# Optimization experiments

Hardware: AMD Instinct MI355X
Metric: run time of the kernel (lower is better)

## Reference

```python
import jax, jax.numpy as jnp
import numpy as np

MODES = 16  # FourierLayer default


def _fourier_layer(h, w):
    # h: [B, S, H] real; w: [H, H, MODES] complex
    S = h.shape[1]
    h_ft = jnp.fft.rfft(h, axis=1)                 # [B, F, H] complex, F = S//2+1
    m = min(MODES, h_ft.shape[1])
    # batched complex matmul over the retained low-frequency modes
    out_m = jnp.einsum('bmh,hkm->bmk', h_ft[:, :m, :], w[:, :, :m])
    out_ft = jnp.zeros_like(h_ft).at[:, :m, :].set(out_m)  # higher modes zeroed
    h = jnp.fft.irfft(out_ft, n=S, axis=1)
    return jax.nn.gelu(h, approximate=False)       # torch nn.GELU() is exact erf


def setup_inputs() -> dict:
    key = jax.random.key(0)
    ks = jax.random.split(key, 7)
    B, S, H, L = 32, 8192, 128, 4
    x = jax.random.normal(ks[0], (B, S), jnp.float32)
    proj_w = jax.random.normal(ks[1], (H,), jnp.float32)          # Linear(1,H).weight[:,0]
    proj_b = jax.random.normal(ks[2], (H,), jnp.float32) * 0.02
    w_re = jax.random.normal(ks[3], (L, H, H, MODES), jnp.float32) * 0.02
    w_im = jax.random.normal(ks[4], (L, H, H, MODES), jnp.float32) * 0.02
    out_w = jax.random.normal(ks[5], (H,), jnp.float32) * 0.02    # Linear(H,1).weight[0]
    out_b = jax.random.normal(ks[6], (1,), jnp.float32) * 0.02
    return {"x": x, "proj_w": proj_w, "proj_b": proj_b,
            "w_re": w_re, "w_im": w_im, "out_w": out_w, "out_b": out_b}


def reference(x, proj_w, proj_b, w_re, w_im, out_w, out_b):
    # projection: Linear(1, H) applied to x.unsqueeze(-1)
    h = x[..., None] * proj_w + proj_b            # [B, S, H]
    W = (w_re + 1j * w_im).astype(jnp.complex64)  # [L, H, H, MODES]
    for l in range(w_re.shape[0]):                # fixed small layer count
        h = _fourier_layer(h, W[l])
    # output projection Linear(H, 1) then squeeze(-1)
    return h @ out_w + out_b[0]                   # [B, S]
```

## Files before the change

kernel.cpp:

```cpp
#include <hip/hip_runtime.h>
#include <hip/hip_bf16.h>

#define S_LEN 8192
#define NH 128
#define NM 16
#define NB 32
#define NBATCH 32
#define GP2 136
#define C2PI 6.2831853071795864769f

typedef __hip_bfloat16 bf16;
typedef unsigned short ushort_t;
typedef unsigned int uint_t;

typedef __bf16 bf16x8 __attribute__((ext_vector_type(8)));
typedef float floatx4 __attribute__((ext_vector_type(4)));

__device__ __forceinline__ float b2f(bf16 v){ return __bfloat162float(v); }
__device__ __forceinline__ float ldf(const void* p, long i, int f32){
    return f32 ? ((const float*)p)[i] : b2f(((const bf16*)p)[i]);
}
__device__ __forceinline__ float gelu_fast(float x){
    float z = fabsf(x) * 0.70710678118654752440f;
    float t = __builtin_amdgcn_rcpf(__builtin_fmaf(0.3275911f, z, 1.0f));
    float p = t*(0.254829592f + t*(-0.284496736f + t*(1.421413741f +
              t*(-1.453152027f + t*1.061405429f))));
    float e = __expf(-z * z);
    float er = __builtin_fmaf(-p, e, 1.0f);
    float s = copysignf(er, x);
    return 0.5f * x * (1.0f + s);
}
__device__ __forceinline__ ushort_t f2us(float v){
    return __builtin_bit_cast(ushort_t, (__bf16)v);
}
__device__ __forceinline__ void split_bf(float v, ushort_t& hi, ushort_t& lo){
    __bf16 h = (__bf16)v;
    float r = v - (float)h;
    hi = __builtin_bit_cast(ushort_t, h);
    lo = __builtin_bit_cast(ushort_t, (__bf16)r);
}
__device__ __forceinline__ bf16x8 ld8(const ushort_t* p){
    return *(const bf16x8*)(const void*)p;
}
__device__ __forceinline__ floatx4 MF(bf16x8 a, bf16x8 b, floatx4 c){
    return __builtin_amdgcn_mfma_f32_16x16x32_bf16(a, b, c, 0, 0, 0);
}

__device__ __forceinline__ int detect_f32(const void* x, int tid){
    __shared__ int sflag;
    if (tid < 64){
        const ushort_t* p = (const ushort_t*)x;
        int cnt = 0;
        for (int i = tid; i < 4096; i += 64){
            int e = (p[i] >> 7) & 0xFF;
            if (e >= 0xA0) cnt++;
        }
        #pragma unroll
        for (int off = 32; off > 0; off >>= 1) cnt += __shfl_xor(cnt, off, 64);
        if (tid == 0) sflag = (cnt > 400) ? 1 : 0;
    }
    __syncthreads();
    return sflag;
}

__device__ __forceinline__ void c_prologue(const float* __restrict__ C,
                                           int b, int c, int q,
                                           bf16x8* Bhi, bf16x8* Blo){
    const float* Cb = C + (long)b * NB * NH;
    #pragma unroll
    for (int kt = 0; kt < 8; kt++){
        int k = kt * 16 + c;
        bf16x8 h8, l8;
        #pragma unroll
        for (int e = 0; e < 8; e++){
            int j = 8 * q + e;
            float sc = (j == 0) ? (1.0f / S_LEN)
                     : (j < NM) ? (2.0f / S_LEN)
                     : (j == NM) ? 0.f : (-2.0f / S_LEN);
            float v = Cb[j * NH + k] * sc;
            __bf16 hh = (__bf16)v;
            h8[e] = hh;
            l8[e] = (__bf16)(v - (float)hh);
        }
        Bhi[kt] = h8; Blo[kt] = l8;
    }
}

__global__ __launch_bounds__(256) void k_prep(const void* __restrict__ x,
                                              const void* __restrict__ pw,
                                              const void* __restrict__ pb,
                                              float* __restrict__ M,
                                              ushort_t* __restrict__ Thi,
                                              ushort_t* __restrict__ Tlo,
                                              ushort_t* __restrict__ TThi,
                                              float* __restrict__ C0){
    int bid = blockIdx.x;
    int tid = threadIdx.x;
    if (bid < 512){
        int f32 = detect_f32(x, tid);
        int m = bid >> 5, b = bid & 31;
        float re = 0.f, im = 0.f;
        for (int s = tid; s < S_LEN; s += 256){
            float xv = ldf(x, (long)b * S_LEN + s, f32);
            float cv = 1.f, sv = 0.f;
            if (m != 0){
                int r = (m * s) & (S_LEN - 1);
                float th = (float)r * (C2PI / (float)S_LEN);
                sincosf(th, &sv, &cv);
            }
            re += xv * cv;
            im -= xv * sv;
        }
        __shared__ float sre[256], sim[256];
        sre[tid] = re; sim[tid] = im;
        __syncthreads();
        for (int off = 128; off > 0; off >>= 1){
            if (tid < off){ sre[tid] += sre[tid + off]; sim[tid] += sim[tid + off]; }
            __syncthreads();
        }
        if (tid < NH){
            float Xre = sre[0], Xim = sim[0];
            int h = tid;
            float pwv = ldf(pw, h, f32);
            float fc = pwv * Xre + (m == 0 ? (float)S_LEN * ldf(pb, h, f32) : 0.f);
            float fs = -pwv * Xim;
            M[(long)b * NB * NH + m * NH + h]        = fc;
            M[(long)b * NB * NH + (NM + m) * NH + h] = fs;
        }
    } else {
        int bb = bid - 512;
        int s = bb * 16 + (tid >> 4);
        int m = tid & 15;
        float cv = 1.f, sv = 0.f;
        if (m != 0){
            int r = (m * s) & (S_LEN - 1);
            float th = (float)r * (C2PI / (float)S_LEN);
            sincosf(th, &sv, &cv);
        }
        ushort_t chi, clo, shi, slo;
        split_bf(cv, chi, clo);
        split_bf(sv, shi, slo);
        Thi[s * NB + m] = chi;       Tlo[s * NB + m] = clo;
        Thi[s * NB + NM + m] = shi;  Tlo[s * NB + NM + m] = slo;
        TThi[m * S_LEN + s] = chi;
        TThi[(NM + m) * S_LEN + s] = shi;
        C0[bb * 256 + tid] = 0.f;
    }
}

__global__ __launch_bounds__(256) void k_mixA(const void* __restrict__ x,
                                              float* __restrict__ M,
                                              const void* __restrict__ wre,
                                              const void* __restrict__ wim,
                                              long woff,
                                              float* __restrict__ C){
    int tid = threadIdx.x;
    int f32 = detect_f32(x, tid);
    int hc = blockIdx.x, b = blockIdx.y;
    int k = tid & 127, mh = tid >> 7;
    int m0 = mh * 8;
    int h0 = hc * 16;
    __shared__ float Ms[NB * 16];
    for (int i = tid; i < NB * 16; i += 256){
        int j = i >> 4, hh = i & 15;
        Ms[j * 16 + hh] = M[(long)b * NB * NH + j * NH + h0 + hh];
    }
    __syncthreads();
    for (int i = tid; i < NB * 16; i += 256){
        int j = i >> 4, hh = i & 15;
        M[(long)b * NB * NH + j * NH + h0 + hh] = 0.f;
    }
    float Cr[8] = {0,0,0,0,0,0,0,0}, Ci[8] = {0,0,0,0,0,0,0,0};
    #pragma unroll 4
    for (int hh = 0; hh < 16; hh++){
        long base = woff + ((long)(h0 + hh) * NH + k) * NM + m0;
        float wr[8], wi[8];
        if (f32){
            const float4* wr4 = (const float4*)((const float*)wre + base);
            const float4* wi4 = (const float4*)((const float*)wim + base);
            float4 a0 = wr4[0], a1 = wr4[1], c0 = wi4[0], c1 = wi4[1];
            wr[0]=a0.x; wr[1]=a0.y; wr[2]=a0.z; wr[3]=a0.w;
            wr[4]=a1.x; wr[5]=a1.y; wr[6]=a1.z; wr[7]=a1.w;
            wi[0]=c0.x; wi[1]=c0.y; wi[2]=c0.z; wi[3]=c0.w;
            wi[4]=c1.x; wi[5]=c1.y; wi[6]=c1.z; wi[7]=c1.w;
        } else {
            bf16x8 a = ld8((const ushort_t*)wre + base);
            bf16x8 c = ld8((const ushort_t*)wim + base);
            #pragma unroll
            for (int e = 0; e < 8; e++){ wr[e] = (float)a[e]; wi[e] = (float)c[e]; }
        }
        #pragma unroll
        for (int e = 0; e < 8; e++){
            float fc = Ms[(m0 + e) * 16 + hh];
            float fs = Ms[(NM + m0 + e) * 16 + hh];
            Cr[e] += fc * wr[e] + fs * wi[e];
            Ci[e] += fc * wi[e] - fs * wr[e];
        }
    }
    float* Cb = C + (long)b * NB * NH;
    #pragma unroll
    for (int e = 0; e < 8; e++){
        atomicAdd(&Cb[(m0 + e) * NH + k],      Cr[e]);
        atomicAdd(&Cb[(NM + m0 + e) * NH + k], Ci[e]);
    }
}

__global__ __launch_bounds__(256, 4) void k_fused(const ushort_t* __restrict__ Thi,
                                                  const ushort_t* __restrict__ Tlo,
                                                  const ushort_t* __restrict__ TThi,
                                                  const float* __restrict__ C,
                                                  float* __restrict__ Cnext,
                                                  float* __restrict__ M){
    int b = blockIdx.y;
    int sx = blockIdx.x;
    int s0 = sx * 256;
    int tid = threadIdx.x;
    int w = tid >> 6;
    int lane = tid & 63;
    int c = lane & 15, q = lane >> 4;
    __shared__ ushort_t Glds[NH * GP2];

    bf16x8 Bhi[8], Blo[8];
    c_prologue(C, b, c, q, Bhi, Blo);
    if (tid < 32){
        *(float4*)(Cnext + (long)b * NB * NH + sx * 128 + tid * 4)
            = (float4){0.f, 0.f, 0.f, 0.f};
    }
    floatx4 a00 = {0,0,0,0}, a01 = {0,0,0,0}, a10 = {0,0,0,0}, a11 = {0,0,0,0};
    int kt0 = 2 * w;
    for (int p = 0; p < 2; p++){
        int sp = s0 + p * 128;
        #pragma unroll
        for (int sti = 0; sti < 2; sti++){
            int st = w * 2 + sti;
            long ar = (long)(sp + st * 16 + c) * NB + 8 * q;
            bf16x8 Ahi = ld8(Thi + ar);
            bf16x8 Alo = ld8(Tlo + ar);
            #pragma unroll
            for (int kt = 0; kt < 8; kt++){
                floatx4 acc = {0.f, 0.f, 0.f, 0.f};
                acc = MF(Ahi, Bhi[kt], acc);
                acc = MF(Alo, Bhi[kt], acc);
                acc = MF(Ahi, Blo[kt], acc);
                uint_t u0 = (uint_t)f2us(gelu_fast(acc[0])) |
                            ((uint_t)f2us(gelu_fast(acc[1])) << 16);
                uint_t u1 = (uint_t)f2us(gelu_fast(acc[2])) |
                            ((uint_t)f2us(gelu_fast(acc[3])) << 16);
                uint_t* gp = (uint_t*)&Glds[(kt * 16 + c) * GP2 + st * 16 + 4 * q];
                gp[0] = u0; gp[1] = u1;
            }
        }
        __syncthreads();
        #pragma unroll
        for (int kk = 0; kk < 4; kk++){
            long sa = (long)sp + kk * 32 + 8 * q;
            bf16x8 A0h = ld8(TThi + (long)c * S_LEN + sa);
            bf16x8 A1h = ld8(TThi + (long)(16 + c) * S_LEN + sa);
            bf16x8 G0 = ld8(&Glds[(kt0 * 16 + c) * GP2 + kk * 32 + 8 * q]);
            bf16x8 G1 = ld8(&Glds[((kt0 + 1) * 16 + c) * GP2 + kk * 32 + 8 * q]);
            a00 = MF(A0h, G0, a00);
            a01 = MF(A0h, G1, a01);
            a10 = MF(A1h, G0, a10);
            a11 = MF(A1h, G1, a11);
        }
        __syncthreads();
    }
    float* Mb = M + (long)b * NB * NH;
    #pragma unroll
    for (int r = 0; r < 4; r++){
        atomicAdd(&Mb[(4 * q + r) * NH + kt0 * 16 + c],            a00[r]);
        atomicAdd(&Mb[(4 * q + r) * NH + (kt0 + 1) * 16 + c],      a01[r]);
        atomicAdd(&Mb[(16 + 4 * q + r) * NH + kt0 * 16 + c],       a10[r]);
        atomicAdd(&Mb[(16 + 4 * q + r) * NH + (kt0 + 1) * 16 + c], a11[r]);
    }
}

__global__ __launch_bounds__(256) void k_final(const void* __restrict__ x,
                                               const ushort_t* __restrict__ Thi,
                                               const ushort_t* __restrict__ Tlo,
                                               const float* __restrict__ C,
                                               const void* __restrict__ ow,
                                               const void* __restrict__ ob,
                                               void* __restrict__ out){
    int tid = threadIdx.x;
    int f32 = detect_f32(x, tid);
    int b = blockIdx.y;
    int s0 = blockIdx.x * 128;
    int w = tid >> 6;
    int lane = tid & 63;
    int c = lane & 15, q = lane >> 4;

    bf16x8 Bhi[8], Blo[8];
    c_prologue(C, b, c, q, Bhi, Blo);
    float ow8[8];
    #pragma unroll
    for (int kt = 0; kt < 8; kt++) ow8[kt] = ldf(ow, kt * 16 + c, f32);
    float obv = ldf(ob, 0, f32);
    #pragma unroll
    for (int sti = 0; sti < 2; sti++){
        int st = w * 2 + sti;
        long ar = (long)(s0 + st * 16 + c) * NB + 8 * q;
        bf16x8 Ahi = ld8(Thi + ar);
        bf16x8 Alo = ld8(Tlo + ar);
        float p0 = 0.f, p1 = 0.f, p2 = 0.f, p3 = 0.f;
        #pragma unroll
        for (int g = 0; g < 2; g++){
            int k0 = g * 4;
            floatx4 ac[4];
            #pragma unroll
            for (int t = 0; t < 4; t++) ac[t] = (floatx4){0.f, 0.f, 0.f, 0.f};
            #pragma unroll
            for (int t = 0; t < 4; t++) ac[t] = MF(Ahi, Bhi[k0 + t], ac[t]);
            #pragma unroll
            for (int t = 0; t < 4; t++) ac[t] = MF(Alo, Bhi[k0 + t], ac[t]);
            #pragma unroll
            for (int t = 0; t < 4; t++) ac[t] = MF(Ahi, Blo[k0 + t], ac[t]);
            #pragma unroll
            for (int t = 0; t < 4; t++){
                float o = ow8[k0 + t];
                p0 += gelu_fast(ac[t][0]) * o;
                p1 += gelu_fast(ac[t][1]) * o;
                p2 += gelu_fast(ac[t][2]) * o;
                p3 += gelu_fast(ac[t][3]) * o;
            }
        }
        #pragma unroll
        for (int off = 1; off < 16; off <<= 1){
            p0 += __shfl_xor(p0, off, 16);
            p1 += __shfl_xor(p1, off, 16);
            p2 += __shfl_xor(p2, off, 16);
            p3 += __shfl_xor(p3, off, 16);
        }
        if (c == 0){
            long s = s0 + st * 16 + 4 * q;
            if (f32){
                float4 v = {p0 + obv, p1 + obv, p2 + obv, p3 + obv};
                *(float4*)((float*)out + (long)b * S_LEN + s) = v;
            } else {
                uint_t u0 = (uint_t)f2us(p0 + obv) | ((uint_t)f2us(p1 + obv) << 16);
                uint_t u1 = (uint_t)f2us(p2 + obv) | ((uint_t)f2us(p3 + obv) << 16);
                uint_t* gp = (uint_t*)((ushort_t*)out + (long)b * S_LEN + s);
                gp[0] = u0; gp[1] = u1;
            }
        }
    }
}

extern "C" void kernel_launch(void* const* d_in, const int* in_sizes, int n_in,
                              void* d_out, int out_size, void* d_ws, size_t ws_size,
                              hipStream_t stream) {
    const void* x   = d_in[0];
    const void* pw  = d_in[1];
    const void* pb  = d_in[2];
    const void* wre = d_in[3];
    const void* wim = d_in[4];
    const void* ow  = d_in[5];
    const void* ob  = d_in[6];

    char* ws = (char*)d_ws;
    ushort_t* Thi  = (ushort_t*)(ws);
    ushort_t* Tlo  = (ushort_t*)(ws + (512u << 10));
    ushort_t* TThi = (ushort_t*)(ws + (1024u << 10));
    float* C0 = (float*)(ws + (1536u << 10));
    float* C1 = (float*)(ws + (2048u << 10));
    float* M  = (float*)d_out;

    k_prep<<<1024, 256, 0, stream>>>(x, pw, pb, M, Thi, Tlo, TThi, C0);

    const long wstride = (long)NH * NH * NM;
    float* Cbuf[2] = {C0, C1};
    for (int l = 0; l < 4; l++){
        float* Ccur = Cbuf[l & 1];
        float* Cnxt = Cbuf[(l + 1) & 1];
        k_mixA<<<dim3(8, NBATCH), 256, 0, stream>>>(x, M, wre, wim,
                                                    l * wstride, Ccur);
        if (l < 3){
            k_fused<<<dim3(32, NBATCH), 256, 0, stream>>>(Thi, Tlo, TThi,
                                                          Ccur, Cnxt, M);
        } else {
            k_final<<<dim3(64, NBATCH), 256, 0, stream>>>(x, Thi, Tlo, Ccur,
                                                          ow, ob, d_out);
        }
    }
}
```

Before: 246.3 us.

## Fuse spectral mode mixing into fused kernel tail via per-batch completion counters

Removes the separate k_mixA launches for layers 1-3. The last 8 blocks per batch to finish k_fused, detected with an atomic counter, spin until all 32 blocks are done and then do the complex weight mixing for the next layer directly. M buffers are ping-ponged and zeroed in the tail, so the zeroing pass in mixA goes away. k_prep switches to hardware sin/cos in revolutions and wave-shuffle reductions. This saves launches and global round trips, but adds spin-wait risk (it needs the blocks to be co-resident) and puts serialized tail work on a few blocks.

New measurement: 428.6 us. 74.1% more time.

```diff
diff --git a/kernel.cpp b/kernel.cpp
--- a/kernel.cpp
+++ b/kernel.cpp
@@ -7,7 +7,6 @@
 #define NB 32
 #define NBATCH 32
 #define GP2 136
-#define C2PI 6.2831853071795864769f
 
 typedef __hip_bfloat16 bf16;
 typedef unsigned short ushort_t;
@@ -93,49 +92,59 @@
                                               ushort_t* __restrict__ Thi,
                                               ushort_t* __restrict__ Tlo,
                                               ushort_t* __restrict__ TThi,
-                                              float* __restrict__ C0){
+                                              float* __restrict__ C0,
+                                              float* __restrict__ MB,
+                                              uint_t* __restrict__ cnt){
     int bid = blockIdx.x;
     int tid = threadIdx.x;
+    int f32 = detect_f32(x, tid);
     if (bid < 512){
-        int f32 = detect_f32(x, tid);
         int m = bid >> 5, b = bid & 31;
         float re = 0.f, im = 0.f;
+        #pragma unroll 4
         for (int s = tid; s < S_LEN; s += 256){
             float xv = ldf(x, (long)b * S_LEN + s, f32);
-            float cv = 1.f, sv = 0.f;
-            if (m != 0){
+            if (m){
                 int r = (m * s) & (S_LEN - 1);
-                float th = (float)r * (C2PI / (float)S_LEN);
-                sincosf(th, &sv, &cv);
+                float rev = (float)r * (1.0f / (float)S_LEN);
+                float sv = __builtin_amdgcn_sinf(rev);
+                float cv = __builtin_amdgcn_cosf(rev);
+                re += xv * cv;
+                im -= xv * sv;
+            } else {
+                re += xv;
             }
-            re += xv * cv;
-            im -= xv * sv;
-        }
-        __shared__ float sre[256], sim[256];
-        sre[tid] = re; sim[tid] = im;
+        }
+        __shared__ float sred[8];
+        #pragma unroll
+        for (int off = 32; off > 0; off >>= 1){
+            re += __shfl_xor(re, off, 64);
+            im += __shfl_xor(im, off, 64);
+        }
+        int w = tid >> 6;
+        if ((tid & 63) == 0){ sred[w] = re; sred[4 + w] = im; }
         __syncthreads();
-        for (int off = 128; off > 0; off >>= 1){
-            if (tid < off){ sre[tid] += sre[tid + off]; sim[tid] += sim[tid + off]; }
-            __syncthreads();
-        }
         if (tid < NH){
-            float Xre = sre[0], Xim = sim[0];
+            float Xre = sred[0] + sred[1] + sred[2] + sred[3];
+            float Xim = sred[4] + sred[5] + sred[6] + sred[7];
             int h = tid;
             float pwv = ldf(pw, h, f32);
             float fc = pwv * Xre + (m == 0 ? (float)S_LEN * ldf(pb, h, f32) : 0.f);
             float fs = -pwv * Xim;
-            M[(long)b * NB * NH + m * NH + h]        = fc;
-            M[(long)b * NB * NH + (NM + m) * NH + h] = fs;
+            float* Mb = M + (long)b * NB * NH;
+            Mb[m * NH + h]        = fc;
+            Mb[(NM + m) * NH + h] = fs;
         }
     } else {
         int bb = bid - 512;
         int s = bb * 16 + (tid >> 4);
         int m = tid & 15;
         float cv = 1.f, sv = 0.f;
-        if (m != 0){
+        if (m){
             int r = (m * s) & (S_LEN - 1);
-            float th = (float)r * (C2PI / (float)S_LEN);
-            sincosf(th, &sv, &cv);
+            float rev = (float)r * (1.0f / (float)S_LEN);
+            sv = __builtin_amdgcn_sinf(rev);
+            cv = __builtin_amdgcn_cosf(rev);
         }
         ushort_t chi, clo, shi, slo;
         split_bf(cv, chi, clo);
@@ -145,35 +154,35 @@
         TThi[m * S_LEN + s] = chi;
         TThi[(NM + m) * S_LEN + s] = shi;
         C0[bb * 256 + tid] = 0.f;
+        MB[bb * 256 + tid] = 0.f;
+        if (bb == 0){
+            if (tid < 96) cnt[tid] = 0u;
+            else if (tid == 96) cnt[96] = (uint_t)f32;
+        }
     }
 }
 
 __global__ __launch_bounds__(256) void k_mixA(const void* __restrict__ x,
-                                              float* __restrict__ M,
+                                              const float* __restrict__ M,
                                               const void* __restrict__ wre,
                                               const void* __restrict__ wim,
-                                              long woff,
                                               float* __restrict__ C){
     int tid = threadIdx.x;
     int f32 = detect_f32(x, tid);
     int hc = blockIdx.x, b = blockIdx.y;
     int k = tid & 127, mh = tid >> 7;
     int m0 = mh * 8;
-    int h0 = hc * 16;
-    __shared__ float Ms[NB * 16];
-    for (int i = tid; i < NB * 16; i += 256){
-        int j = i >> 4, hh = i & 15;
-        Ms[j * 16 + hh] = M[(long)b * NB * NH + j * NH + h0 + hh];
-    }
-    __syncthreads();
-    for (int i = tid; i < NB * 16; i += 256){
-        int j = i >> 4, hh = i & 15;
-        M[(long)b * NB * NH + j * NH + h0 + hh] = 0.f;
-    }
+    int h0 = hc * 8;
+    __shared__ float Ms[NB * 8];
+    {
+        int j = tid >> 3, hh = tid & 7;
+        Ms[tid] = M[(long)b * NB * NH + j * NH + h0 + hh];
+    }
+    __syncthreads();
     float Cr[8] = {0,0,0,0,0,0,0,0}, Ci[8] = {0,0,0,0,0,0,0,0};
     #pragma unroll 4
-    for (int hh = 0; hh < 16; hh++){
-        long base = woff + ((long)(h0 + hh) * NH + k) * NM + m0;
+    for (int hh = 0; hh < 8; hh++){
+        long base = ((long)(h0 + hh) * NH + k) * NM + m0;
         float wr[8], wi[8];
         if (f32){
             const float4* wr4 = (const float4*)((const float*)wre + base);
@@ -191,8 +200,8 @@
         }
         #pragma unroll
         for (int e = 0; e < 8; e++){
-            float fc = Ms[(m0 + e) * 16 + hh];
-            float fs = Ms[(NM + m0 + e) * 16 + hh];
+            float fc = Ms[(m0 + e) * 8 + hh];
+            float fs = Ms[(NM + m0 + e) * 8 + hh];
             Cr[e] += fc * wr[e] + fs * wi[e];
             Ci[e] += fc * wi[e] - fs * wr[e];
         }
@@ -210,7 +219,13 @@
                                                   const ushort_t* __restrict__ TThi,
                                                   const float* __restrict__ C,
                                                   float* __restrict__ Cnext,
-                                                  float* __restrict__ M){
+                                                  float* __restrict__ Macc,
+                                                  float* __restrict__ Mdead,
+                                                  const void* __restrict__ wre,
+                                                  const void* __restrict__ wim,
+                                                  long wnext,
+                                                  uint_t* __restrict__ cntL,
+                                                  const uint_t* __restrict__ flagp){
     int b = blockIdx.y;
     int sx = blockIdx.x;
     int s0 = sx * 256;
@@ -218,14 +233,11 @@
     int w = tid >> 6;
     int lane = tid & 63;
     int c = lane & 15, q = lane >> 4;
-    __shared__ ushort_t Glds[NH * GP2];
+    __shared__ __align__(16) ushort_t Glds[NH * GP2];
+    __shared__ uint_t sOld;
 
     bf16x8 Bhi[8], Blo[8];
     c_prologue(C, b, c, q, Bhi, Blo);
-    if (tid < 32){
-        *(float4*)(Cnext + (long)b * NB * NH + sx * 128 + tid * 4)
-            = (float4){0.f, 0.f, 0.f, 0.f};
-    }
     floatx4 a00 = {0,0,0,0}, a01 = {0,0,0,0}, a10 = {0,0,0,0}, a11 = {0,0,0,0};
     int kt0 = 2 * w;
     for (int p = 0; p < 2; p++){
@@ -265,13 +277,93 @@
         }
         __syncthreads();
     }
-    float* Mb = M + (long)b * NB * NH;
+    float* Mb = Macc + (long)b * NB * NH;
     #pragma unroll
     for (int r = 0; r < 4; r++){
         atomicAdd(&Mb[(4 * q + r) * NH + kt0 * 16 + c],            a00[r]);
         atomicAdd(&Mb[(4 * q + r) * NH + (kt0 + 1) * 16 + c],      a01[r]);
         atomicAdd(&Mb[(16 + 4 * q + r) * NH + kt0 * 16 + c],       a10[r]);
         atomicAdd(&Mb[(16 + 4 * q + r) * NH + (kt0 + 1) * 16 + c], a11[r]);
+    }
+
+    __syncthreads();
+    if (tid == 0){
+        sOld = __hip_atomic_fetch_add(&cntL[b], 1u, __ATOMIC_RELEASE,
+                                      __HIP_MEMORY_SCOPE_AGENT);
+    }
+    __syncthreads();
+    uint_t old = sOld;
+    if (old < 24u) return;
+    int idx = (int)old - 24;
+    if (tid == 0){
+        while (__hip_atomic_fetch_add(&cntL[b], 0u, __ATOMIC_RELAXED,
+                                      __HIP_MEMORY_SCOPE_AGENT) < 32u)
+            __builtin_amdgcn_s_sleep(2);
+    }
+    __syncthreads();
+    float* Msl = (float*)Glds;
+    float* Macb = Macc + (long)b * NB * NH;
+    #pragma unroll
+    for (int t = 0; t < 16; t++){
+        int i = tid + t * 256;
+        Msl[i] = __hip_atomic_fetch_add(Macb + i, 0.f, __ATOMIC_RELAXED,
+                                        __HIP_MEMORY_SCOPE_AGENT);
+    }
+    if (Mdead){
+        float* Mdb = Mdead + (long)b * NB * NH;
+        for (int t = tid; t < 512; t += 256) Mdb[idx * 512 + t] = 0.f;
+    }
+    __syncthreads();
+    int kk = tid & 15, mg = (tid >> 4) & 3, wv = tid >> 6;
+    int k = idx * 16 + kk;
+    int f32 = (int)flagp[0];
+    float Cr[4] = {0,0,0,0}, Ci[4] = {0,0,0,0};
+    for (int hq = 0; hq < 32; hq++){
+        int h = wv * 32 + hq;
+        long base = wnext + ((long)h * NH + k) * NM + 4 * mg;
+        float wr4[4], wi4[4];
+        if (f32){
+            float4 a  = *(const float4*)((const float*)wre + base);
+            float4 cc = *(const float4*)((const float*)wim + base);
+            wr4[0]=a.x;  wr4[1]=a.y;  wr4[2]=a.z;  wr4[3]=a.w;
+            wi4[0]=cc.x; wi4[1]=cc.y; wi4[2]=cc.z; wi4[3]=cc.w;
+        } else {
+            ushort4 a  = *(const ushort4*)((const ushort_t*)wre + base);
+            ushort4 cc = *(const ushort4*)((const ushort_t*)wim + base);
+            wr4[0]=b2f(__builtin_bit_cast(bf16, a.x));
+            wr4[1]=b2f(__builtin_bit_cast(bf16, a.y));
+            wr4[2]=b2f(__builtin_bit_cast(bf16, a.z));
+            wr4[3]=b2f(__builtin_bit_cast(bf16, a.w));
+            wi4[0]=b2f(__builtin_bit_cast(bf16, cc.x));
+            wi4[1]=b2f(__builtin_bit_cast(bf16, cc.y));
+            wi4[2]=b2f(__builtin_bit_cast(bf16, cc.z));
+            wi4[3]=b2f(__builtin_bit_cast(bf16, cc.w));
+        }
+        #pragma unroll
+        for (int e = 0; e < 4; e++){
+            float fc = Msl[(4 * mg + e) * NH + h];
+            float fs = Msl[(NM + 4 * mg + e) * NH + h];
+            Cr[e] += fc * wr4[e] + fs * wi4[e];
+            Ci[e] += fc * wi4[e] - fs * wr4[e];
+        }
+    }
+    float* redr = Msl + 4096;
+    float* redi = redr + 1024;
+    __syncthreads();
+    #pragma unroll
+    for (int e = 0; e < 4; e++){
+        redr[wv * 256 + (4 * mg + e) * 16 + kk] = Cr[e];
+        redi[wv * 256 + (4 * mg + e) * 16 + kk] = Ci[e];
+    }
+    __syncthreads();
+    {
+        int m = tid >> 4, k2 = tid & 15;
+        int o = m * 16 + k2;
+        float sr = redr[o] + redr[256 + o] + redr[512 + o] + redr[768 + o];
+        float si = redi[o] + redi[256 + o] + redi[512 + o] + redi[768 + o];
+        float* Cnb = Cnext + (long)b * NB * NH;
+        Cnb[m * NH + idx * 16 + k2]        = sr;
+        Cnb[(NM + m) * NH + idx * 16 + k2] = si;
     }
 }
 
@@ -363,23 +455,22 @@
     ushort_t* TThi = (ushort_t*)(ws + (1024u << 10));
     float* C0 = (float*)(ws + (1536u << 10));
     float* C1 = (float*)(ws + (2048u << 10));
-    float* M  = (float*)d_out;
-
-    k_prep<<<1024, 256, 0, stream>>>(x, pw, pb, M, Thi, Tlo, TThi, C0);
+    float* MB = (float*)(ws + (2560u << 10));
+    uint_t* cnt = (uint_t*)(ws + (3072u << 10));
+    float* MA = (float*)d_out;
 
     const long wstride = (long)NH * NH * NM;
-    float* Cbuf[2] = {C0, C1};
-    for (int l = 0; l < 4; l++){
-        float* Ccur = Cbuf[l & 1];
-        float* Cnxt = Cbuf[(l + 1) & 1];
-        k_mixA<<<dim3(8, NBATCH), 256, 0, stream>>>(x, M, wre, wim,
-                                                    l * wstride, Ccur);
-        if (l < 3){
-            k_fused<<<dim3(32, NBATCH), 256, 0, stream>>>(Thi, Tlo, TThi,
-                                                          Ccur, Cnxt, M);
-        } else {
-            k_final<<<dim3(64, NBATCH), 256, 0, stream>>>(x, Thi, Tlo, Ccur,
-                                                          ow, ob, d_out);
-        }
-    }
-}
+
+    k_prep<<<1024, 256, 0, stream>>>(x, pw, pb, MA, Thi, Tlo, TThi, C0, MB, cnt);
+    k_mixA<<<dim3(16, NBATCH), 256, 0, stream>>>(x, MA, wre, wim, C0);
+    k_fused<<<dim3(32, NBATCH), 256, 0, stream>>>(Thi, Tlo, TThi, C0, C1,
+                                                  MB, MA, wre, wim,
+                                                  1 * wstride, cnt +  0, cnt + 96);
+    k_fused<<<dim3(32, NBATCH), 256, 0, stream>>>(Thi, Tlo, TThi, C1, C0,
+                                                  MA, MB, wre, wim,
+                                                  2 * wstride, cnt + 32, cnt + 96);
+    k_fused<<<dim3(32, NBATCH), 256, 0, stream>>>(Thi, Tlo, TThi, C0, C1,
+                                                  MB, (float*)0, wre, wim,
+                                                  3 * wstride, cnt + 64, cnt + 96);
+    k_final<<<dim3(64, NBATCH), 256, 0, stream>>>(x, Thi, Tlo, C1, ow, ob, d_out);
+}
```

## Replace atomic mode accumulation with per-block partial buffers and hardware sin/cos

Applied to the files above, without the earlier changes.

k_fused now writes its per-block mode projections to a partial buffer indexed by block instead of issuing atomicAdd into a shared M array, and k_mixA sums the 32 partials itself while loading. This removes atomic contention and the separate zeroing of M. k_prep uses the hardware sin/cos builtins (which take revolutions) instead of sincosf, and a wavefront shuffle reduction instead of a shared-memory tree. In exchange, k_mixA reads 32 times more M data per block and uses extra workspace.

Result: slower. 281.0 us (+14.1%).

```diff
diff --git a/kernel.cpp b/kernel.cpp
--- a/kernel.cpp
+++ b/kernel.cpp
@@ -7,7 +7,6 @@
 #define NB 32
 #define NBATCH 32
 #define GP2 136
-#define C2PI 6.2831853071795864769f
 
 typedef __hip_bfloat16 bf16;
 typedef unsigned short ushort_t;
@@ -96,46 +95,54 @@
                                               float* __restrict__ C0){
     int bid = blockIdx.x;
     int tid = threadIdx.x;
+    int f32 = detect_f32(x, tid);
     if (bid < 512){
-        int f32 = detect_f32(x, tid);
         int m = bid >> 5, b = bid & 31;
         float re = 0.f, im = 0.f;
+        #pragma unroll 4
         for (int s = tid; s < S_LEN; s += 256){
             float xv = ldf(x, (long)b * S_LEN + s, f32);
-            float cv = 1.f, sv = 0.f;
-            if (m != 0){
+            if (m){
                 int r = (m * s) & (S_LEN - 1);
-                float th = (float)r * (C2PI / (float)S_LEN);
-                sincosf(th, &sv, &cv);
+                float rev = (float)r * (1.0f / (float)S_LEN);
+                float sv = __builtin_amdgcn_sinf(rev);
+                float cv = __builtin_amdgcn_cosf(rev);
+                re += xv * cv;
+                im -= xv * sv;
+            } else {
+                re += xv;
             }
-            re += xv * cv;
-            im -= xv * sv;
-        }
-        __shared__ float sre[256], sim[256];
-        sre[tid] = re; sim[tid] = im;
+        }
+        __shared__ float sred[8];
+        #pragma unroll
+        for (int off = 32; off > 0; off >>= 1){
+            re += __shfl_xor(re, off, 64);
+            im += __shfl_xor(im, off, 64);
+        }
+        int w = tid >> 6;
+        if ((tid & 63) == 0){ sred[w] = re; sred[4 + w] = im; }
         __syncthreads();
-        for (int off = 128; off > 0; off >>= 1){
-            if (tid < off){ sre[tid] += sre[tid + off]; sim[tid] += sim[tid + off]; }
-            __syncthreads();
-        }
         if (tid < NH){
-            float Xre = sre[0], Xim = sim[0];
+            float Xre = sred[0] + sred[1] + sred[2] + sred[3];
+            float Xim = sred[4] + sred[5] + sred[6] + sred[7];
             int h = tid;
             float pwv = ldf(pw, h, f32);
             float fc = pwv * Xre + (m == 0 ? (float)S_LEN * ldf(pb, h, f32) : 0.f);
             float fs = -pwv * Xim;
-            M[(long)b * NB * NH + m * NH + h]        = fc;
-            M[(long)b * NB * NH + (NM + m) * NH + h] = fs;
+            float* Mb = M + (long)b * NB * NH;
+            Mb[m * NH + h]        = fc;
+            Mb[(NM + m) * NH + h] = fs;
         }
     } else {
         int bb = bid - 512;
         int s = bb * 16 + (tid >> 4);
         int m = tid & 15;
         float cv = 1.f, sv = 0.f;
-        if (m != 0){
+        if (m){
             int r = (m * s) & (S_LEN - 1);
-            float th = (float)r * (C2PI / (float)S_LEN);
-            sincosf(th, &sv, &cv);
+            float rev = (float)r * (1.0f / (float)S_LEN);
+            sv = __builtin_amdgcn_sinf(rev);
+            cv = __builtin_amdgcn_cosf(rev);
         }
         ushort_t chi, clo, shi, slo;
         split_bf(cv, chi, clo);
@@ -149,7 +156,8 @@
 }
 
 __global__ __launch_bounds__(256) void k_mixA(const void* __restrict__ x,
-                                              float* __restrict__ M,
+                                              const float* __restrict__ Msrc,
+                                              int nparts,
                                               const void* __restrict__ wre,
                                               const void* __restrict__ wim,
                                               long woff,
@@ -163,13 +171,12 @@
     __shared__ float Ms[NB * 16];
     for (int i = tid; i < NB * 16; i += 256){
         int j = i >> 4, hh = i & 15;
-        Ms[j * 16 + hh] = M[(long)b * NB * NH + j * NH + h0 + hh];
+        const float* mp = Msrc + (long)b * nparts * (NB * NH) + j * NH + h0 + hh;
+        float acc = 0.f;
+        for (int sx = 0; sx < nparts; sx++) acc += mp[(long)sx * NB * NH];
+        Ms[j * 16 + hh] = acc;
     }
     __syncthreads();
-    for (int i = tid; i < NB * 16; i += 256){
-        int j = i >> 4, hh = i & 15;
-        M[(long)b * NB * NH + j * NH + h0 + hh] = 0.f;
-    }
     float Cr[8] = {0,0,0,0,0,0,0,0}, Ci[8] = {0,0,0,0,0,0,0,0};
     #pragma unroll 4
     for (int hh = 0; hh < 16; hh++){
@@ -210,7 +217,7 @@
                                                   const ushort_t* __restrict__ TThi,
                                                   const float* __restrict__ C,
                                                   float* __restrict__ Cnext,
-                                                  float* __restrict__ M){
+                                                  float* __restrict__ Mpart){
     int b = blockIdx.y;
     int sx = blockIdx.x;
     int s0 = sx * 256;
@@ -218,7 +225,7 @@
     int w = tid >> 6;
     int lane = tid & 63;
     int c = lane & 15, q = lane >> 4;
-    __shared__ ushort_t Glds[NH * GP2];
+    __shared__ __align__(16) ushort_t Glds[NH * GP2];
 
     bf16x8 Bhi[8], Blo[8];
     c_prologue(C, b, c, q, Bhi, Blo);
@@ -265,13 +272,13 @@
         }
         __syncthreads();
     }
-    float* Mb = M + (long)b * NB * NH;
+    float* Mb = Mpart + ((long)b * 32 + sx) * (NB * NH);
     #pragma unroll
     for (int r = 0; r < 4; r++){
-        atomicAdd(&Mb[(4 * q + r) * NH + kt0 * 16 + c],            a00[r]);
-        atomicAdd(&Mb[(4 * q + r) * NH + (kt0 + 1) * 16 + c],      a01[r]);
-        atomicAdd(&Mb[(16 + 4 * q + r) * NH + kt0 * 16 + c],       a10[r]);
-        atomicAdd(&Mb[(16 + 4 * q + r) * NH + (kt0 + 1) * 16 + c], a11[r]);
+        Mb[(4 * q + r) * NH + kt0 * 16 + c]            = a00[r];
+        Mb[(4 * q + r) * NH + (kt0 + 1) * 16 + c]      = a01[r];
+        Mb[(16 + 4 * q + r) * NH + kt0 * 16 + c]       = a10[r];
+        Mb[(16 + 4 * q + r) * NH + (kt0 + 1) * 16 + c] = a11[r];
     }
 }
 
@@ -361,25 +368,24 @@
     ushort_t* Thi  = (ushort_t*)(ws);
     ushort_t* Tlo  = (ushort_t*)(ws + (512u << 10));
     ushort_t* TThi = (ushort_t*)(ws + (1024u << 10));
-    float* C0 = (float*)(ws + (1536u << 10));
-    float* C1 = (float*)(ws + (2048u << 10));
-    float* M  = (float*)d_out;
-
-    k_prep<<<1024, 256, 0, stream>>>(x, pw, pb, M, Thi, Tlo, TThi, C0);
+    float* C0    = (float*)(ws + (1536u << 10));
+    float* C1    = (float*)(ws + (2048u << 10));
+    float* Mfull = (float*)(ws + (2560u << 10));
+    float* Mpart = (float*)(ws + (3072u << 10));
 
     const long wstride = (long)NH * NH * NM;
-    float* Cbuf[2] = {C0, C1};
-    for (int l = 0; l < 4; l++){
-        float* Ccur = Cbuf[l & 1];
-        float* Cnxt = Cbuf[(l + 1) & 1];
-        k_mixA<<<dim3(8, NBATCH), 256, 0, stream>>>(x, M, wre, wim,
-                                                    l * wstride, Ccur);
-        if (l < 3){
-            k_fused<<<dim3(32, NBATCH), 256, 0, stream>>>(Thi, Tlo, TThi,
-                                                          Ccur, Cnxt, M);
-        } else {
-            k_final<<<dim3(64, NBATCH), 256, 0, stream>>>(x, Thi, Tlo, Ccur,
-                                                          ow, ob, d_out);
-        }
-    }
-}
+
+    k_prep<<<1024, 256, 0, stream>>>(x, pw, pb, Mfull, Thi, Tlo, TThi, C0);
+    k_mixA<<<dim3(8, NBATCH), 256, 0, stream>>>(x, Mfull, 1, wre, wim,
+                                                0 * wstride, C0);
+    k_fused<<<dim3(32, NBATCH), 256, 0, stream>>>(Thi, Tlo, TThi, C0, C1, Mpart);
+    k_mixA<<<dim3(8, NBATCH), 256, 0, stream>>>(x, Mpart, 32, wre, wim,
+                                                1 * wstride, C1);
+    k_fused<<<dim3(32, NBATCH), 256, 0, stream>>>(Thi, Tlo, TThi, C1, C0, Mpart);
+    k_mixA<<<dim3(8, NBATCH), 256, 0, stream>>>(x, Mpart, 32, wre, wim,
+                                                2 * wstride, C0);
+    k_fused<<<dim3(32, NBATCH), 256, 0, stream>>>(Thi, Tlo, TThi, C0, C1, Mpart);
+    k_mixA<<<dim3(8, NBATCH), 256, 0, stream>>>(x, Mpart, 32, wre, wim,
+                                                3 * wstride, C1);
+    k_final<<<dim3(64, NBATCH), 256, 0, stream>>>(x, Thi, Tlo, C1, ow, ob, d_out);
+}
```
